# Performance work log

Hardware: AMD Instinct MI355X
Metric: run time of the kernel (lower is better)

## Reference

```python
import jax, jax.numpy as jnp
import numpy as np

MIN_POS = 1e-6
EPS = 1e-20
B, S, F_IN, E, H = 2, 1024, 768, 768, 12
DH = E // H   # nnmf in_features per head (64)
FH = E // H   # nnmf out_features per head (hidden_features=embed_dim default)
N_NNMF_ITERS = 3
N_ALPHA_ITERS = 3


def l1norm(x, axis=-1):
    # F.normalize(x, p=1, dim=axis, eps=1e-20) for non-negative x
    return x / jnp.maximum(jnp.sum(jnp.abs(x), axis=axis, keepdims=True), EPS)


def setup_inputs() -> dict:
    key = jax.random.key(0)
    k = jax.random.split(key, 6)
    return {
        "x": jax.random.normal(k[0], (B, S, F_IN), jnp.float32),
        "embed_w": jax.random.normal(k[1], (E, F_IN), jnp.float32) * 0.02,
        "embed_b": jnp.zeros((E,), jnp.float32),
        "nnmf_w": jax.random.uniform(k[2], (FH, DH), jnp.float32),  # non-negative NMF dictionary
        "out_w": jax.random.normal(k[3], (F_IN, E), jnp.float32) * 0.02,
        "out_b": jnp.zeros((F_IN,), jnp.float32),
    }


def reference(x, embed_w, embed_b, nnmf_w, out_w, out_b):
    # normalize NMF weight rows (p=1 over in_features), as nnmf_layer.normalize_weights
    W = nnmf_w / jnp.maximum(jnp.sum(nnmf_w, axis=1, keepdims=True), EPS)  # [FH, DH]

    # embed + clamp positive, split heads
    xe = jnp.clip(x @ embed_w.T + embed_b, MIN_POS)            # [B,S,E]
    xe = xe.reshape(B, S, H, DH)                                # [B,S,H,DH]

    # NNMFDense: prepared_input = l1-normalized input (normalize_input_dim=-1)
    inp = l1norm(xe)                                            # [B,S,H,DH]
    h = l1norm(jnp.ones((B, S, H, FH), x.dtype))                # init hidden
    rec = inp
    for _ in range(N_NNMF_ITERS):
        rec = l1norm(jnp.clip(h @ W, MIN_POS))                  # reconstruction [B,S,H,DH]
        h = l1norm(jnp.clip(h * ((inp / rec) @ W.T), MIN_POS))  # multiplicative update

    # normalize_h (p=1, dim=-1)
    h = l1norm(h)                                               # [B,S,H,FH] -> 'bohf'

    # alpha dynamics fixed point
    alpha = jnp.ones((B, H, S, S), x.dtype)                     # 'bhoi'
    h_rec_input = rec * inp                                     # [B,S,H,DH]
    for _ in range(N_ALPHA_ITERS):
        h_mixed = jnp.einsum('bohf,bhoi->bihf', h, alpha)       # [B,S,H,FH]
        arec_inv = 1.0 / (h_mixed @ W + EPS)                    # _reconstruct -> [B,S,H,DH]
        alpha = alpha * jnp.einsum('bohf,bihf->bhoi', h_rec_input, arec_inv)

    out = jnp.einsum('bohf,bhoi->bihf', h, alpha)               # [B,S,H,FH]
    out = out.reshape(B, S, E)                                  # flatten heads
    return out @ out_w.T + out_b                                # out_project
```

## Files before the change

### kernel.cpp

```cpp
#include <hip/hip_runtime.h>

#define B_  2
#define S_  1024
#define FIN 768
#define E_  768
#define H_  12
#define DH  64

typedef unsigned int uint;
typedef unsigned short ushort;
typedef __attribute__((ext_vector_type(8))) short short8;
typedef __attribute__((ext_vector_type(4))) float floatx4;

__device__ __forceinline__ ushort f2bf(float f) {
    uint u = __float_as_uint(f);
    return (ushort)((u + 0x7fffu + ((u >> 16) & 1u)) >> 16);
}

__device__ __forceinline__ uint4 pack8(const ushort* p) {
    uint4 r;
    r.x = (uint)p[0] | ((uint)p[1] << 16);
    r.y = (uint)p[2] | ((uint)p[3] << 16);
    r.z = (uint)p[4] | ((uint)p[5] << 16);
    r.w = (uint)p[6] | ((uint)p[7] << 16);
    return r;
}

__device__ __forceinline__ void split8v(float4 a, float4 b, short8& hi, short8& lo) {
    float v[8] = {a.x, a.y, a.z, a.w, b.x, b.y, b.z, b.w};
    ushort h[8], l[8];
#pragma unroll
    for (int j = 0; j < 8; ++j) {
        h[j] = f2bf(v[j]);
        l[j] = f2bf(v[j] - __uint_as_float(((uint)h[j]) << 16));
    }
    uint4 H = pack8(h), L = pack8(l);
    hi = *(short8*)&H;
    lo = *(short8*)&L;
}

__global__ __launch_bounds__(256) void k_embed_prep(const float* __restrict__ xs,
                                                    const float* __restrict__ ew,
                                                    const float* __restrict__ eb,
                                                    const float* __restrict__ nw,
                                                    float* __restrict__ Wn,
                                                    float* __restrict__ WnT,
                                                    float* __restrict__ r1inv,
                                                    float* __restrict__ zbase,
                                                    float* __restrict__ inp) {
    __shared__ __align__(16) unsigned char smem[28160];
    const int tid = threadIdx.x;
    const int bid = blockIdx.x;

    if (bid >= 768) {
        const int pb = bid - 768;
        if (pb == 0) {
            float* Wl = (float*)smem;
            const int f = tid >> 2, q = tid & 3;
            float v[16];
            float s = 0.f;
#pragma unroll
            for (int i = 0; i < 16; ++i) { v[i] = nw[f * 64 + q * 16 + i]; s += v[i]; }
            s += __shfl_xor(s, 1, 64);
            s += __shfl_xor(s, 2, 64);
            const float inv = 1.f / fmaxf(s, 1e-20f);
#pragma unroll
            for (int i = 0; i < 16; ++i) {
                float w = v[i] * inv;
                Wn[f * 64 + q * 16 + i] = w;
                WnT[(q * 16 + i) * 64 + f] = w;
                Wl[f * 65 + q * 16 + i] = w;
            }
            __syncthreads();
            if (tid < 64) {
                float cs = 0.f;
                for (int ff = 0; ff < 64; ++ff) cs += Wl[ff * 65 + tid];
                float t = fmaxf(cs * (1.f / 64.f), 1e-6f);
                float S = t;
#pragma unroll
                for (int m = 1; m < 64; m <<= 1) S += __shfl_xor(S, m, 64);
                S = fmaxf(S, 1e-20f);
                r1inv[tid] = S / t;
            }
        } else {
            const int i = (pb - 1) * 1024 + tid * 4;
            if (i < 26112) {
                float4 z = make_float4(0.f, 0.f, 0.f, 0.f);
                *(float4*)(zbase + i) = z;
            }
        }
        return;
    }

    const int head = bid % 12;
    const int tok0 = (bid / 12) * 32;
    ushort* As_hi = (ushort*)smem;
    ushort* As_lo = As_hi + 32 * 72;
    ushort* Bs_hi = As_lo + 32 * 72;
    ushort* Bs_lo = Bs_hi + 64 * 72;
    float*  RS    = (float*)(Bs_lo + 64 * 72);

    const int wv = tid >> 6, lane = tid & 63;
    const int mbase = (wv >> 1) * 16;
    const int nbase = (wv & 1) * 32;
    const int lm = lane & 15, lq = lane >> 4;

    floatx4 acc[2];
    acc[0] = (floatx4)0.f;
    acc[1] = (floatx4)0.f;

    const int arow = tid >> 3, akc = (tid & 7) * 8;
    const int brow = tid >> 2, bkq = (tid & 3) * 16;
    const float* xrow = xs + (size_t)(tok0 + arow) * FIN + akc;
    const float* wrg  = ew + (size_t)(head * 64 + brow) * FIN + bkq;

    float4 pa[2], pb[4];
#pragma unroll
    for (int c = 0; c < 2; ++c) pa[c] = *(const float4*)(xrow + c * 4);
#pragma unroll
    for (int c = 0; c < 4; ++c) pb[c] = *(const float4*)(wrg + c * 4);

    for (int kb = 0; kb < FIN; kb += 64) {
        __syncthreads();
        {
            ushort ah[8], al[8], bh[16], bl[16];
            float va[8] = {pa[0].x, pa[0].y, pa[0].z, pa[0].w,
                           pa[1].x, pa[1].y, pa[1].z, pa[1].w};
#pragma unroll
            for (int j = 0; j < 8; ++j) {
                ah[j] = f2bf(va[j]);
                al[j] = f2bf(va[j] - __uint_as_float(((uint)ah[j]) << 16));
            }
#pragma unroll
            for (int c4 = 0; c4 < 4; ++c4) {
                float vb[4] = {pb[c4].x, pb[c4].y, pb[c4].z, pb[c4].w};
#pragma unroll
                for (int j = 0; j < 4; ++j) {
                    ushort g = f2bf(vb[j]);
                    bh[c4 * 4 + j] = g;
                    bl[c4 * 4 + j] = f2bf(vb[j] - __uint_as_float(((uint)g) << 16));
                }
            }
            const int aoff = arow * 72 + akc;
            *(uint4*)&As_hi[aoff] = pack8(ah);
            *(uint4*)&As_lo[aoff] = pack8(al);
            const int boff = brow * 72 + bkq;
            *(uint4*)&Bs_hi[boff]     = pack8(bh);
            *(uint4*)&Bs_hi[boff + 8] = pack8(bh + 8);
            *(uint4*)&Bs_lo[boff]     = pack8(bl);
            *(uint4*)&Bs_lo[boff + 8] = pack8(bl + 8);
        }
        __syncthreads();
        if (kb + 64 < FIN) {
#pragma unroll
            for (int c = 0; c < 2; ++c) pa[c] = *(const float4*)(xrow + kb + 64 + c * 4);
#pragma unroll
            for (int c = 0; c < 4; ++c) pb[c] = *(const float4*)(wrg + kb + 64 + c * 4);
        }
#pragma unroll
        for (int ch = 0; ch < 2; ++ch) {
            const int ko = ch * 32 + lq * 8;
            short8 ah = *(const short8*)&As_hi[(mbase + lm) * 72 + ko];
            short8 al = *(const short8*)&As_lo[(mbase + lm) * 72 + ko];
#pragma unroll
            for (int ti = 0; ti < 2; ++ti) {
                short8 bh = *(const short8*)&Bs_hi[(nbase + ti * 16 + lm) * 72 + ko];
                short8 bl = *(const short8*)&Bs_lo[(nbase + ti * 16 + lm) * 72 + ko];
                acc[ti] = __builtin_amdgcn_mfma_f32_16x16x32_bf16(ah, bh, acc[ti], 0, 0, 0);
                acc[ti] = __builtin_amdgcn_mfma_f32_16x16x32_bf16(al, bh, acc[ti], 0, 0, 0);
                acc[ti] = __builtin_amdgcn_mfma_f32_16x16x32_bf16(ah, bl, acc[ti], 0, 0, 0);
            }
        }
    }

    const float b0 = eb[head * 64 + nbase + lm];
    const float b1 = eb[head * 64 + nbase + 16 + lm];
    float xe[2][4];
    float rs[4];
#pragma unroll
    for (int r = 0; r < 4; ++r) {
        float e0 = fmaxf(acc[0][r] + b0, 1e-6f);
        float e1 = fmaxf(acc[1][r] + b1, 1e-6f);
        xe[0][r] = e0; xe[1][r] = e1;
        float p = e0 + e1;
        p += __shfl_xor(p, 1, 64);
        p += __shfl_xor(p, 2, 64);
        p += __shfl_xor(p, 4, 64);
        p += __shfl_xor(p, 8, 64);
        rs[r] = p;
    }
    if (lm == 0) {
#pragma unroll
        for (int r = 0; r < 4; ++r)
            RS[(wv & 1) * 32 + mbase + lq * 4 + r] = rs[r];
    }
    __syncthreads();
    const size_t obase = ((size_t)((tok0 >> 10) * 12 + head) * 1024 + (tok0 & 1023));
#pragma unroll
    for (int r = 0; r < 4; ++r) {
        const int m = mbase + lq * 4 + r;
        const float inv = 1.f / fmaxf(RS[m] + RS[32 + m], 1e-20f);
        float* op = inp + (obase + m) * 64;
        op[nbase + lm]      = xe[0][r] * inv;
        op[nbase + 16 + lm] = xe[1][r] * inv;
    }
}

__device__ __forceinline__ void mfma_matvec(const float srcC[4][4], float* T,
                                            int lm, int lq,
                                            const ushort* WH, const ushort* WL,
                                            floatx4 out[4]) {
    __builtin_amdgcn_wave_barrier();
#pragma unroll
    for (int nt = 0; nt < 4; ++nt)
#pragma unroll
        for (int r = 0; r < 4; ++r)
            T[(lq * 4 + r) * 68 + nt * 16 + lm] = srcC[nt][r];
    __builtin_amdgcn_wave_barrier();
    float4 a00 = *(const float4*)&T[lm * 68 + lq * 8];
    float4 a01 = *(const float4*)&T[lm * 68 + lq * 8 + 4];
    float4 a10 = *(const float4*)&T[lm * 68 + 32 + lq * 8];
    float4 a11 = *(const float4*)&T[lm * 68 + 32 + lq * 8 + 4];
    __builtin_amdgcn_wave_barrier();
    short8 A0h, A0l, A1h, A1l;
    split8v(a00, a01, A0h, A0l);
    split8v(a10, a11, A1h, A1l);
#pragma unroll
    for (int nt = 0; nt < 4; ++nt) {
        const int row = (nt * 16 + lm) * 72;
        short8 b0h = *(const short8*)&WH[row + lq * 8];
        short8 b0l = *(const short8*)&WL[row + lq * 8];
        short8 b1h = *(const short8*)&WH[row + 32 + lq * 8];
        short8 b1l = *(const short8*)&WL[row + 32 + lq * 8];
        floatx4 acc = (floatx4)0.f;
        acc = __builtin_amdgcn_mfma_f32_16x16x32_bf16(A0h, b0h, acc, 0, 0, 0);
        acc = __builtin_amdgcn_mfma_f32_16x16x32_bf16(A0l, b0h, acc, 0, 0, 0);
        acc = __builtin_amdgcn_mfma_f32_16x16x32_bf16(A0h, b0l, acc, 0, 0, 0);
        acc = __builtin_amdgcn_mfma_f32_16x16x32_bf16(A1h, b1h, acc, 0, 0, 0);
        acc = __builtin_amdgcn_mfma_f32_16x16x32_bf16(A1l, b1h, acc, 0, 0, 0);
        acc = __builtin_amdgcn_mfma_f32_16x16x32_bf16(A1h, b1l, acc, 0, 0, 0);
        out[nt] = acc;
    }
}

__global__ __launch_bounds__(256) void k_nnmf(const float* __restrict__ inp,
                                              const float* __restrict__ Wn,
                                              const float* __restrict__ WnT,
                                              const float* __restrict__ r1inv,
                                              float* __restrict__ hout,
                                              float* __restrict__ hriout,
                                              float* __restrict__ mp0) {
    __shared__ ushort WtH[64 * 72], WtL[64 * 72];
    __shared__ ushort WwH[64 * 72], WwL[64 * 72];
    __shared__ float Tb[4][16 * 68];
    const int tid = threadIdx.x, wv = tid >> 6, lane = tid & 63;
    const int lm = lane & 15, lq = lane >> 4;
    float* T = Tb[wv];
    const int rowbase = blockIdx.x * 64 + wv * 16;

    {
        const int row = tid >> 2, kq = (tid & 3) * 16;
        short8 h0, l0, h1, l1;
        split8v(*(const float4*)(WnT + row * 64 + kq), *(const float4*)(WnT + row * 64 + kq + 4), h0, l0);
        split8v(*(const float4*)(WnT + row * 64 + kq + 8), *(const float4*)(WnT + row * 64 + kq + 12), h1, l1);
        *(short8*)&WtH[row * 72 + kq] = h0; *(short8*)&WtH[row * 72 + kq + 8] = h1;
        *(short8*)&WtL[row * 72 + kq] = l0; *(short8*)&WtL[row * 72 + kq + 8] = l1;
        split8v(*(const float4*)(Wn + row * 64 + kq), *(const float4*)(Wn + row * 64 + kq + 4), h0, l0);
        split8v(*(const float4*)(Wn + row * 64 + kq + 8), *(const float4*)(Wn + row * 64 + kq + 12), h1, l1);
        *(short8*)&WwH[row * 72 + kq] = h0; *(short8*)&WwH[row * 72 + kq + 8] = h1;
        *(short8*)&WwL[row * 72 + kq] = l0; *(short8*)&WwL[row * 72 + kq + 8] = l1;
    }

    float inpC[4][4];
#pragma unroll
    for (int nt = 0; nt < 4; ++nt)
#pragma unroll
        for (int r = 0; r < 4; ++r)
            inpC[nt][r] = inp[(size_t)(rowbase + lq * 4 + r) * 64 + nt * 16 + lm];
    float r1c[4];
#pragma unroll
    for (int nt = 0; nt < 4; ++nt) r1c[nt] = r1inv[nt * 16 + lm];
    __syncthreads();

    float hC[4][4], recC[4][4];
    {
        float qC[4][4];
#pragma unroll
        for (int nt = 0; nt < 4; ++nt)
#pragma unroll
            for (int r = 0; r < 4; ++r) qC[nt][r] = inpC[nt][r] * r1c[nt];
        floatx4 u[4];
        mfma_matvec(qC, T, lm, lq, WwH, WwL, u);
#pragma unroll
        for (int nt = 0; nt < 4; ++nt)
#pragma unroll
            for (int r = 0; r < 4; ++r)
                hC[nt][r] = fmaxf(u[nt][r] * (1.f / 64.f), 1e-6f);
#pragma unroll
        for (int r = 0; r < 4; ++r) {
            float s = (hC[0][r] + hC[1][r]) + (hC[2][r] + hC[3][r]);
            s += __shfl_xor(s, 1, 64); s += __shfl_xor(s, 2, 64);
            s += __shfl_xor(s, 4, 64); s += __shfl_xor(s, 8, 64);
            const float inv = __builtin_amdgcn_rcpf(fmaxf(s, 1e-20f));
#pragma unroll
            for (int nt = 0; nt < 4; ++nt) hC[nt][r] *= inv;
        }
    }
#pragma unroll 1
    for (int it = 0; it < 2; ++it) {
        floatx4 t[4];
        mfma_matvec(hC, T, lm, lq, WtH, WtL, t);
        float tC[4][4], qC[4][4];
#pragma unroll
        for (int nt = 0; nt < 4; ++nt)
#pragma unroll
            for (int r = 0; r < 4; ++r) tC[nt][r] = fmaxf(t[nt][r], 1e-6f);
#pragma unroll
        for (int r = 0; r < 4; ++r) {
            float s = (tC[0][r] + tC[1][r]) + (tC[2][r] + tC[3][r]);
            s += __shfl_xor(s, 1, 64); s += __shfl_xor(s, 2, 64);
            s += __shfl_xor(s, 4, 64); s += __shfl_xor(s, 8, 64);
            s = fmaxf(s, 1e-20f);
            const float invS = __builtin_amdgcn_rcpf(s);
#pragma unroll
            for (int nt = 0; nt < 4; ++nt) {
                recC[nt][r] = tC[nt][r] * invS;
                qC[nt][r] = inpC[nt][r] * s * __builtin_amdgcn_rcpf(tC[nt][r]);
            }
        }
        floatx4 u[4];
        mfma_matvec(qC, T, lm, lq, WwH, WwL, u);
#pragma unroll
        for (int nt = 0; nt < 4; ++nt)
#pragma unroll
            for (int r = 0; r < 4; ++r)
                hC[nt][r] = fmaxf(hC[nt][r] * u[nt][r], 1e-6f);
#pragma unroll
        for (int r = 0; r < 4; ++r) {
            float s = (hC[0][r] + hC[1][r]) + (hC[2][r] + hC[3][r]);
            s += __shfl_xor(s, 1, 64); s += __shfl_xor(s, 2, 64);
            s += __shfl_xor(s, 4, 64); s += __shfl_xor(s, 8, 64);
            const float inv = __builtin_amdgcn_rcpf(fmaxf(s, 1e-20f));
#pragma unroll
            for (int nt = 0; nt < 4; ++nt) hC[nt][r] *= inv;
        }
    }
#pragma unroll
    for (int r = 0; r < 4; ++r) {
        float s = (hC[0][r] + hC[1][r]) + (hC[2][r] + hC[3][r]);
        s += __shfl_xor(s, 1, 64); s += __shfl_xor(s, 2, 64);
        s += __shfl_xor(s, 4, 64); s += __shfl_xor(s, 8, 64);
        const float inv = __builtin_amdgcn_rcpf(fmaxf(s, 1e-20f));
#pragma unroll
        for (int nt = 0; nt < 4; ++nt) hC[nt][r] *= inv;
    }
#pragma unroll
    for (int nt = 0; nt < 4; ++nt)
#pragma unroll
        for (int r = 0; r < 4; ++r) {
            const size_t o = (size_t)(rowbase + lq * 4 + r) * 64 + nt * 16 + lm;
            hout[o] = hC[nt][r];
            hriout[o] = recC[nt][r] * inpC[nt][r];
        }
    float hs[4];
#pragma unroll
    for (int nt = 0; nt < 4; ++nt) {
        float s = (hC[nt][0] + hC[nt][1]) + (hC[nt][2] + hC[nt][3]);
        s += __shfl_xor(s, 16, 64);
        s += __shfl_xor(s, 32, 64);
        hs[nt] = s;
    }
    float mvv = lq == 0 ? hs[0] : lq == 1 ? hs[1] : lq == 2 ? hs[2] : hs[3];
    atomicAdd(&mp0[(size_t)blockIdx.x * 64 + lq * 16 + lm], mvv);
}

__global__ __launch_bounds__(256) void k_alpha_step(const float* __restrict__ hin,
                                                    const float* __restrict__ hri,
                                                    const float* __restrict__ Wn,
                                                    const float* __restrict__ mp_in,
                                                    float* __restrict__ mp_out,
                                                    float* __restrict__ c,
                                                    float* __restrict__ M,
                                                    int it) {
    __shared__ float mred[4][64];
    __shared__ float mv[64];
    __shared__ float vv[64];
    __shared__ float cl[64];
    const int tid = threadIdx.x;
    const int bh = blockIdx.x >> 4;
    const int chunk = blockIdx.x & 15;
    const size_t rowbase = (size_t)bh * 1024 + chunk * 64;

    {
        int f = tid & 63, p = tid >> 6;
        float s = 0.f;
#pragma unroll
        for (int pp = 0; pp < 4; ++pp)
            s += mp_in[((size_t)bh * 16 + p * 4 + pp) * 64 + f];
        mred[p][f] = s;
    }
    __syncthreads();
    if (tid < 64)
        mv[tid] = (mred[0][tid] + mred[1][tid]) + (mred[2][tid] + mred[3][tid]);
    __syncthreads();
    {
        int d = tid & 63, qq = tid >> 6;
        float r = 0.f;
#pragma unroll
        for (int ff = 0; ff < 16; ++ff)
            r = fmaf(mv[qq * 16 + ff], Wn[(size_t)(qq * 16 + ff) * 64 + d], r);
        mred[qq][d] = r;
    }
    __syncthreads();
    if (tid < 64)
        vv[tid] = 1.f / (((mred[0][tid] + mred[1][tid]) + (mred[2][tid] + mred[3][tid])) + 1e-20f);
    __syncthreads();
    {
        int o = tid >> 2, dq = tid & 3;
        const float* rp = hri + (rowbase + o) * 64 + dq * 16;
        float dot = 0.f;
#pragma unroll
        for (int t4 = 0; t4 < 16; t4 += 4) {
            float4 r4 = *(const float4*)(rp + t4);
            dot = fmaf(r4.x, vv[dq * 16 + t4 + 0], dot);
            dot = fmaf(r4.y, vv[dq * 16 + t4 + 1], dot);
            dot = fmaf(r4.z, vv[dq * 16 + t4 + 2], dot);
            dot = fmaf(r4.w, vv[dq * 16 + t4 + 3], dot);
        }
        dot += __shfl_xor(dot, 1, 64);
        dot += __shfl_xor(dot, 2, 64);
        float cn = dot;
        if (it >= 2) cn *= c[rowbase + o];
        if (dq == 0) { c[rowbase + o] = cn; cl[o] = cn; }
    }
    __syncthreads();
    {
        const int f4 = (tid & 15) * 4, ogr = tid >> 4;
        float4 a = make_float4(0.f, 0.f, 0.f, 0.f);
#pragma unroll
        for (int oi = 0; oi < 4; ++oi) {
            int o = ogr * 4 + oi;
            float4 h4 = *(const float4*)(hin + (rowbase + o) * 64 + f4);
            float cv = cl[o];
            a.x = fmaf(h4.x, cv, a.x); a.y = fmaf(h4.y, cv, a.y);
            a.z = fmaf(h4.z, cv, a.z); a.w = fmaf(h4.w, cv, a.w);
        }
        a.x += __shfl_xor(a.x, 16, 64); a.y += __shfl_xor(a.y, 16, 64);
        a.z += __shfl_xor(a.z, 16, 64); a.w += __shfl_xor(a.w, 16, 64);
        a.x += __shfl_xor(a.x, 32, 64); a.y += __shfl_xor(a.y, 32, 64);
        a.z += __shfl_xor(a.z, 32, 64); a.w += __shfl_xor(a.w, 32, 64);
        const int w = tid >> 6;
        if ((tid & 63) < 16) *(float4*)&mred[w][(tid & 15) * 4] = a;
    }
    __syncthreads();
    if (tid < 64) {
        float s = (mred[0][tid] + mred[1][tid]) + (mred[2][tid] + mred[3][tid]);
        if (it == 3) atomicAdd(&M[(size_t)bh * 64 + tid], s);
        else mp_out[((size_t)bh * 16 + chunk) * 64 + tid] = s;
    }
}

__global__ __launch_bounds__(256) void k_projbcast(const float* __restrict__ M,
                                                   const float* __restrict__ ow,
                                                   const float* __restrict__ ob,
                                                   float* __restrict__ out) {
    __shared__ float Ml[768];
    __shared__ float ps[4][64];
    __shared__ float yseg[64];
    const int tid = threadIdx.x;
    const int b = blockIdx.x / 192;
    const int rem = blockIdx.x - b * 192;
    const int jt = rem >> 4, rg = rem & 15;
    for (int i = tid; i < 768; i += 256) Ml[i] = M[b * 768 + i];
    __syncthreads();
    const int jj = tid & 63, part = tid >> 6;
    const int j = jt * 64 + jj;
    const float* row = ow + (size_t)j * 768 + part * 192;
    float acc = 0.f;
    for (int t = 0; t < 192; t += 4) {
        float4 w4 = *(const float4*)(row + t);
        acc = fmaf(w4.x, Ml[part * 192 + t + 0], acc);
        acc = fmaf(w4.y, Ml[part * 192 + t + 1], acc);
        acc = fmaf(w4.z, Ml[part * 192 + t + 2], acc);
        acc = fmaf(w4.w, Ml[part * 192 + t + 3], acc);
    }
    ps[part][jj] = acc;
    __syncthreads();
    if (tid < 64)
        yseg[tid] = ps[0][tid] + ps[1][tid] + ps[2][tid] + ps[3][tid] + ob[jt * 64 + tid];
    __syncthreads();
    const int r0 = tid >> 2, c4 = (tid & 3) * 16;
    float4 v4[4];
#pragma unroll
    for (int q = 0; q < 4; ++q) v4[q] = *(const float4*)&yseg[c4 + q * 4];
    float* dst = out + ((size_t)(b * 1024 + rg * 64 + r0)) * 768 + jt * 64 + c4;
#pragma unroll
    for (int q = 0; q < 4; ++q) *(float4*)(dst + q * 4) = v4[q];
}

extern "C" void kernel_launch(void* const* d_in, const int* in_sizes, int n_in,
                              void* d_out, int out_size, void* d_ws, size_t ws_size,
                              hipStream_t stream) {
    const float* xs = (const float*)d_in[0];
    const float* ew = (const float*)d_in[1];
    const float* eb = (const float*)d_in[2];
    const float* nw = (const float*)d_in[3];
    const float* ow = (const float*)d_in[4];
    const float* ob = (const float*)d_in[5];
    float* out = (float*)d_out;

    float* ws    = (float*)d_ws;
    float* inp   = ws;
    float* h     = ws + 1572864;
    float* hri   = ws + 3145728;
    float* Wn    = ws + 4718592;
    float* WnT   = ws + 4722688;
    float* r1inv = ws + 4726784;
    float* mp0   = ws + 4727040;
    float* M     = ws + 4751616;
    float* mp1   = ws + 4753152;
    float* mp2   = ws + 4777728;
    float* c     = ws + 4802304;

    k_embed_prep<<<795, 256, 0, stream>>>(xs, ew, eb, nw, Wn, WnT, r1inv, mp0, inp);
    k_nnmf<<<384, 256, 0, stream>>>(inp, Wn, WnT, r1inv, h, hri, mp0);
    k_alpha_step<<<384, 256, 0, stream>>>(h, hri, Wn, mp0, mp1, c, M, 1);
    k_alpha_step<<<384, 256, 0, stream>>>(h, hri, Wn, mp1, mp2, c, M, 2);
    k_alpha_step<<<384, 256, 0, stream>>>(h, hri, Wn, mp2, mp1, c, M, 3);
    k_projbcast<<<384, 256, 0, stream>>>(M, ow, ob, out);
}
```

Measured before the change: 132.0 us.

## Fuse three alpha-step launches into one per-head kernel with transposed h layout

```diff
diff --git a/kernel.cpp b/kernel.cpp
--- a/kernel.cpp
+++ b/kernel.cpp
@@ -46,48 +46,38 @@
                                                     float* __restrict__ Wn,
                                                     float* __restrict__ WnT,
                                                     float* __restrict__ r1inv,
-                                                    float* __restrict__ zbase,
                                                     float* __restrict__ inp) {
     __shared__ __align__(16) unsigned char smem[28160];
     const int tid = threadIdx.x;
     const int bid = blockIdx.x;
 
     if (bid >= 768) {
-        const int pb = bid - 768;
-        if (pb == 0) {
-            float* Wl = (float*)smem;
-            const int f = tid >> 2, q = tid & 3;
-            float v[16];
-            float s = 0.f;
-#pragma unroll
-            for (int i = 0; i < 16; ++i) { v[i] = nw[f * 64 + q * 16 + i]; s += v[i]; }
-            s += __shfl_xor(s, 1, 64);
-            s += __shfl_xor(s, 2, 64);
-            const float inv = 1.f / fmaxf(s, 1e-20f);
-#pragma unroll
-            for (int i = 0; i < 16; ++i) {
-                float w = v[i] * inv;
-                Wn[f * 64 + q * 16 + i] = w;
-                WnT[(q * 16 + i) * 64 + f] = w;
-                Wl[f * 65 + q * 16 + i] = w;
-            }
-            __syncthreads();
-            if (tid < 64) {
-                float cs = 0.f;
-                for (int ff = 0; ff < 64; ++ff) cs += Wl[ff * 65 + tid];
-                float t = fmaxf(cs * (1.f / 64.f), 1e-6f);
-                float S = t;
-#pragma unroll
-                for (int m = 1; m < 64; m <<= 1) S += __shfl_xor(S, m, 64);
-                S = fmaxf(S, 1e-20f);
-                r1inv[tid] = S / t;
-            }
-        } else {
-            const int i = (pb - 1) * 1024 + tid * 4;
-            if (i < 26112) {
-                float4 z = make_float4(0.f, 0.f, 0.f, 0.f);
-                *(float4*)(zbase + i) = z;
-            }
+        float* Wl = (float*)smem;
+        const int f = tid >> 2, q = tid & 3;
+        float v[16];
+        float s = 0.f;
+#pragma unroll
+        for (int i = 0; i < 16; ++i) { v[i] = nw[f * 64 + q * 16 + i]; s += v[i]; }
+        s += __shfl_xor(s, 1, 64);
+        s += __shfl_xor(s, 2, 64);
+        const float inv = 1.f / fmaxf(s, 1e-20f);
+#pragma unroll
+        for (int i = 0; i < 16; ++i) {
+            float w = v[i] * inv;
+            Wn[f * 64 + q * 16 + i] = w;
+            WnT[(q * 16 + i) * 64 + f] = w;
+            Wl[f * 65 + q * 16 + i] = w;
+        }
+        __syncthreads();
+        if (tid < 64) {
+            float cs = 0.f;
+            for (int ff = 0; ff < 64; ++ff) cs += Wl[ff * 65 + tid];
+            float t = fmaxf(cs * (1.f / 64.f), 1e-6f);
+            float S = t;
+#pragma unroll
+            for (int m = 1; m < 64; m <<= 1) S += __shfl_xor(S, m, 64);
+            S = fmaxf(S, 1e-20f);
+            r1inv[tid] = S / t;
         }
         return;
     }
@@ -247,8 +237,8 @@
                                               const float* __restrict__ Wn,
                                               const float* __restrict__ WnT,
                                               const float* __restrict__ r1inv,
-                                              float* __restrict__ hout,
-                                              float* __restrict__ hriout,
+                                              float* __restrict__ hT,
+                                              float* __restrict__ hriT,
                                               float* __restrict__ mp0) {
     __shared__ ushort WtH[64 * 72], WtL[64 * 72];
     __shared__ ushort WwH[64 * 72], WwL[64 * 72];
@@ -354,14 +344,7 @@
 #pragma unroll
         for (int nt = 0; nt < 4; ++nt) hC[nt][r] *= inv;
     }
-#pragma unroll
-    for (int nt = 0; nt < 4; ++nt)
-#pragma unroll
-        for (int r = 0; r < 4; ++r) {
-            const size_t o = (size_t)(rowbase + lq * 4 + r) * 64 + nt * 16 + lm;
-            hout[o] = hC[nt][r];
-            hriout[o] = recC[nt][r] * inpC[nt][r];
-        }
+
     float hs[4];
 #pragma unroll
     for (int nt = 0; nt < 4; ++nt) {
@@ -370,93 +353,131 @@
         s += __shfl_xor(s, 32, 64);
         hs[nt] = s;
     }
-    float mvv = lq == 0 ? hs[0] : lq == 1 ? hs[1] : lq == 2 ? hs[2] : hs[3];
-    atomicAdd(&mp0[(size_t)blockIdx.x * 64 + lq * 16 + lm], mvv);
-}
-
-__global__ __launch_bounds__(256) void k_alpha_step(const float* __restrict__ hin,
-                                                    const float* __restrict__ hri,
-                                                    const float* __restrict__ Wn,
-                                                    const float* __restrict__ mp_in,
-                                                    float* __restrict__ mp_out,
-                                                    float* __restrict__ c,
-                                                    float* __restrict__ M,
-                                                    int it) {
-    __shared__ float mred[4][64];
-    __shared__ float mv[64];
-    __shared__ float vv[64];
-    __shared__ float cl[64];
-    const int tid = threadIdx.x;
-    const int bh = blockIdx.x >> 4;
-    const int chunk = blockIdx.x & 15;
-    const size_t rowbase = (size_t)bh * 1024 + chunk * 64;
-
-    {
-        int f = tid & 63, p = tid >> 6;
+
+    __syncthreads();
+    float* TBh = (float*)WwH;
+    float* TBr = (float*)WtH;
+    float* pbuf = (float*)Tb;
+#pragma unroll
+    for (int nt = 0; nt < 4; ++nt)
+#pragma unroll
+        for (int r = 0; r < 4; ++r) {
+            const int ol = wv * 16 + lq * 4 + r, f = nt * 16 + lm;
+            TBh[ol * 65 + f] = hC[nt][r];
+            TBr[ol * 65 + f] = recC[nt][r] * inpC[nt][r];
+        }
+    pbuf[wv * 64 + lq * 16 + lm] = hs[lq];
+    __syncthreads();
+    const int bh = blockIdx.x >> 4, obase = (blockIdx.x & 15) * 64;
+    float* hTb  = hT   + (size_t)bh * 64 * 1024 + obase;
+    float* rTb  = hriT + (size_t)bh * 64 * 1024 + obase;
+#pragma unroll
+    for (int p = 0; p < 16; ++p) {
+        const int f = wv * 16 + p;
+        hTb[(size_t)f * 1024 + lane] = TBh[lane * 65 + f];
+        rTb[(size_t)f * 1024 + lane] = TBr[lane * 65 + f];
+    }
+    if (tid < 64) {
+        float tot = (pbuf[tid] + pbuf[64 + tid]) + (pbuf[128 + tid] + pbuf[192 + tid]);
+        mp0[(size_t)blockIdx.x * 64 + tid] = tot;
+    }
+}
+
+__global__ __launch_bounds__(1024) void k_alpha(const float* __restrict__ hT,
+                                                const float* __restrict__ hriT,
+                                                const float* __restrict__ Wn,
+                                                const float* __restrict__ mp0,
+                                                float* __restrict__ M) {
+    __shared__ float red[16 * 64];
+    __shared__ float mvl[64];
+    __shared__ float vvl[64];
+    __shared__ float cl[1024];
+    const int tid = threadIdx.x, bh = blockIdx.x;
+    const int w = tid >> 6, lane = tid & 63;
+    const float* hTb = hT   + (size_t)bh * 64 * 1024;
+    const float* rTb = hriT + (size_t)bh * 64 * 1024;
+
+    float rT[64];
+#pragma unroll
+    for (int f = 0; f < 64; ++f) rT[f] = rTb[(size_t)f * 1024 + tid];
+    float wcol[4];
+#pragma unroll
+    for (int j = 0; j < 4; ++j) wcol[j] = Wn[(size_t)(w * 4 + j) * 64 + lane];
+
+    float c = 1.f;
+#pragma unroll 1
+    for (int it = 1; it <= 3; ++it) {
+        if (it == 1) {
+            red[tid] = mp0[((size_t)bh * 16 + w) * 64 + lane];
+            __syncthreads();
+            if (tid < 64) {
+                float s = 0.f;
+#pragma unroll
+                for (int cc = 0; cc < 16; ++cc) s += red[cc * 64 + tid];
+                mvl[tid] = s;
+            }
+        } else {
+#pragma unroll
+            for (int j = 0; j < 4; ++j) {
+                const int f = w * 4 + j;
+                const float* hrow = hTb + (size_t)f * 1024;
+                float s = 0.f;
+#pragma unroll
+                for (int k = 0; k < 4; ++k) {
+                    const float4 hv = *(const float4*)(hrow + lane * 4 + k * 256);
+                    const float4 cv = *(const float4*)&cl[lane * 4 + k * 256];
+                    s = fmaf(hv.x, cv.x, s); s = fmaf(hv.y, cv.y, s);
+                    s = fmaf(hv.z, cv.z, s); s = fmaf(hv.w, cv.w, s);
+                }
+                s += __shfl_xor(s, 1, 64);  s += __shfl_xor(s, 2, 64);
+                s += __shfl_xor(s, 4, 64);  s += __shfl_xor(s, 8, 64);
+                s += __shfl_xor(s, 16, 64); s += __shfl_xor(s, 32, 64);
+                if (lane == 0) mvl[f] = s;
+            }
+        }
+        __syncthreads();
+        {
+            float r = 0.f;
+#pragma unroll
+            for (int j = 0; j < 4; ++j) r = fmaf(mvl[w * 4 + j], wcol[j], r);
+            red[tid] = r;
+        }
+        __syncthreads();
+        if (tid < 64) {
+            float s = 0.f;
+#pragma unroll
+            for (int cc = 0; cc < 16; ++cc) s += red[cc * 64 + tid];
+            vvl[tid] = 1.f / (s + 1e-20f);
+        }
+        __syncthreads();
+        float d0 = 0.f, d1 = 0.f, d2 = 0.f, d3 = 0.f;
+#pragma unroll
+        for (int f = 0; f < 64; f += 4) {
+            d0 = fmaf(rT[f + 0], vvl[f + 0], d0);
+            d1 = fmaf(rT[f + 1], vvl[f + 1], d1);
+            d2 = fmaf(rT[f + 2], vvl[f + 2], d2);
+            d3 = fmaf(rT[f + 3], vvl[f + 3], d3);
+        }
+        c *= ((d0 + d1) + (d2 + d3));
+        cl[tid] = c;
+        __syncthreads();
+    }
+#pragma unroll
+    for (int j = 0; j < 4; ++j) {
+        const int f = w * 4 + j;
+        const float* hrow = hTb + (size_t)f * 1024;
         float s = 0.f;
 #pragma unroll
-        for (int pp = 0; pp < 4; ++pp)
-            s += mp_in[((size_t)bh * 16 + p * 4 + pp) * 64 + f];
-        mred[p][f] = s;
-    }
-    __syncthreads();
-    if (tid < 64)
-        mv[tid] = (mred[0][tid] + mred[1][tid]) + (mred[2][tid] + mred[3][tid]);
-    __syncthreads();
-    {
-        int d = tid & 63, qq = tid >> 6;
-        float r = 0.f;
-#pragma unroll
-        for (int ff = 0; ff < 16; ++ff)
-            r = fmaf(mv[qq * 16 + ff], Wn[(size_t)(qq * 16 + ff) * 64 + d], r);
-        mred[qq][d] = r;
-    }
-    __syncthreads();
-    if (tid < 64)
-        vv[tid] = 1.f / (((mred[0][tid] + mred[1][tid]) + (mred[2][tid] + mred[3][tid])) + 1e-20f);
-    __syncthreads();
-    {
-        int o = tid >> 2, dq = tid & 3;
-        const float* rp = hri + (rowbase + o) * 64 + dq * 16;
-        float dot = 0.f;
-#pragma unroll
-        for (int t4 = 0; t4 < 16; t4 += 4) {
-            float4 r4 = *(const float4*)(rp + t4);
-            dot = fmaf(r4.x, vv[dq * 16 + t4 + 0], dot);
-            dot = fmaf(r4.y, vv[dq * 16 + t4 + 1], dot);
-            dot = fmaf(r4.z, vv[dq * 16 + t4 + 2], dot);
-            dot = fmaf(r4.w, vv[dq * 16 + t4 + 3], dot);
-        }
-        dot += __shfl_xor(dot, 1, 64);
-        dot += __shfl_xor(dot, 2, 64);
-        float cn = dot;
-        if (it >= 2) cn *= c[rowbase + o];
-        if (dq == 0) { c[rowbase + o] = cn; cl[o] = cn; }
-    }
-    __syncthreads();
-    {
-        const int f4 = (tid & 15) * 4, ogr = tid >> 4;
-        float4 a = make_float4(0.f, 0.f, 0.f, 0.f);
-#pragma unroll
-        for (int oi = 0; oi < 4; ++oi) {
-            int o = ogr * 4 + oi;
-            float4 h4 = *(const float4*)(hin + (rowbase + o) * 64 + f4);
-            float cv = cl[o];
-            a.x = fmaf(h4.x, cv, a.x); a.y = fmaf(h4.y, cv, a.y);
-            a.z = fmaf(h4.z, cv, a.z); a.w = fmaf(h4.w, cv, a.w);
-        }
-        a.x += __shfl_xor(a.x, 16, 64); a.y += __shfl_xor(a.y, 16, 64);
-        a.z += __shfl_xor(a.z, 16, 64); a.w += __shfl_xor(a.w, 16, 64);
-        a.x += __shfl_xor(a.x, 32, 64); a.y += __shfl_xor(a.y, 32, 64);
-        a.z += __shfl_xor(a.z, 32, 64); a.w += __shfl_xor(a.w, 32, 64);
-        const int w = tid >> 6;
-        if ((tid & 63) < 16) *(float4*)&mred[w][(tid & 15) * 4] = a;
-    }
-    __syncthreads();
-    if (tid < 64) {
-        float s = (mred[0][tid] + mred[1][tid]) + (mred[2][tid] + mred[3][tid]);
-        if (it == 3) atomicAdd(&M[(size_t)bh * 64 + tid], s);
-        else mp_out[((size_t)bh * 16 + chunk) * 64 + tid] = s;
+        for (int k = 0; k < 4; ++k) {
+            const float4 hv = *(const float4*)(hrow + lane * 4 + k * 256);
+            const float4 cv = *(const float4*)&cl[lane * 4 + k * 256];
+            s = fmaf(hv.x, cv.x, s); s = fmaf(hv.y, cv.y, s);
+            s = fmaf(hv.z, cv.z, s); s = fmaf(hv.w, cv.w, s);
+        }
+        s += __shfl_xor(s, 1, 64);  s += __shfl_xor(s, 2, 64);
+        s += __shfl_xor(s, 4, 64);  s += __shfl_xor(s, 8, 64);
+        s += __shfl_xor(s, 16, 64); s += __shfl_xor(s, 32, 64);
+        if (lane == 0) M[(size_t)bh * 64 + f] = s;
     }
 }
 
@@ -511,21 +532,16 @@
 
     float* ws    = (float*)d_ws;
     float* inp   = ws;
-    float* h     = ws + 1572864;
-    float* hri   = ws + 3145728;
+    float* hT    = ws + 1572864;
+    float* hriT  = ws + 3145728;
     float* Wn    = ws + 4718592;
     float* WnT   = ws + 4722688;
     float* r1inv = ws + 4726784;
     float* mp0   = ws + 4727040;
     float* M     = ws + 4751616;
-    float* mp1   = ws + 4753152;
-    float* mp2   = ws + 4777728;
-    float* c     = ws + 4802304;
-
-    k_embed_prep<<<795, 256, 0, stream>>>(xs, ew, eb, nw, Wn, WnT, r1inv, mp0, inp);
-    k_nnmf<<<384, 256, 0, stream>>>(inp, Wn, WnT, r1inv, h, hri, mp0);
-    k_alpha_step<<<384, 256, 0, stream>>>(h, hri, Wn, mp0, mp1, c, M, 1);
-    k_alpha_step<<<384, 256, 0, stream>>>(h, hri, Wn, mp1, mp2, c, M, 2);
-    k_alpha_step<<<384, 256, 0, stream>>>(h, hri, Wn, mp2, mp1, c, M, 3);
+
+    k_embed_prep<<<769, 256, 0, stream>>>(xs, ew, eb, nw, Wn, WnT, r1inv, inp);
+    k_nnmf<<<384, 256, 0, stream>>>(inp, Wn, WnT, r1inv, hT, hriT, mp0);
+    k_alpha<<<24, 1024, 0, stream>>>(hT, hriT, Wn, mp0, M);
     k_projbcast<<<384, 256, 0, stream>>>(M, ow, ob, out);
 }
```

Result: slower. 137.5 us (+4.1%).

## Replace atomics and zero-init with deterministic partial sums; split MFMA accumulators

Applied to the files above, without the earlier changes.

```diff
diff --git a/kernel.cpp b/kernel.cpp
--- a/kernel.cpp
+++ b/kernel.cpp
@@ -46,48 +46,38 @@
                                                     float* __restrict__ Wn,
                                                     float* __restrict__ WnT,
                                                     float* __restrict__ r1inv,
-                                                    float* __restrict__ zbase,
                                                     float* __restrict__ inp) {
     __shared__ __align__(16) unsigned char smem[28160];
     const int tid = threadIdx.x;
     const int bid = blockIdx.x;
 
     if (bid >= 768) {
-        const int pb = bid - 768;
-        if (pb == 0) {
-            float* Wl = (float*)smem;
-            const int f = tid >> 2, q = tid & 3;
-            float v[16];
-            float s = 0.f;
-#pragma unroll
-            for (int i = 0; i < 16; ++i) { v[i] = nw[f * 64 + q * 16 + i]; s += v[i]; }
-            s += __shfl_xor(s, 1, 64);
-            s += __shfl_xor(s, 2, 64);
-            const float inv = 1.f / fmaxf(s, 1e-20f);
-#pragma unroll
-            for (int i = 0; i < 16; ++i) {
-                float w = v[i] * inv;
-                Wn[f * 64 + q * 16 + i] = w;
-                WnT[(q * 16 + i) * 64 + f] = w;
-                Wl[f * 65 + q * 16 + i] = w;
-            }
-            __syncthreads();
-            if (tid < 64) {
-                float cs = 0.f;
-                for (int ff = 0; ff < 64; ++ff) cs += Wl[ff * 65 + tid];
-                float t = fmaxf(cs * (1.f / 64.f), 1e-6f);
-                float S = t;
-#pragma unroll
-                for (int m = 1; m < 64; m <<= 1) S += __shfl_xor(S, m, 64);
-                S = fmaxf(S, 1e-20f);
-                r1inv[tid] = S / t;
-            }
-        } else {
-            const int i = (pb - 1) * 1024 + tid * 4;
-            if (i < 26112) {
-                float4 z = make_float4(0.f, 0.f, 0.f, 0.f);
-                *(float4*)(zbase + i) = z;
-            }
+        float* Wl = (float*)smem;
+        const int f = tid >> 2, q = tid & 3;
+        float v[16];
+        float s = 0.f;
+#pragma unroll
+        for (int i = 0; i < 16; ++i) { v[i] = nw[f * 64 + q * 16 + i]; s += v[i]; }
+        s += __shfl_xor(s, 1, 64);
+        s += __shfl_xor(s, 2, 64);
+        const float inv = 1.f / fmaxf(s, 1e-20f);
+#pragma unroll
+        for (int i = 0; i < 16; ++i) {
+            float w = v[i] * inv;
+            Wn[f * 64 + q * 16 + i] = w;
+            WnT[(q * 16 + i) * 64 + f] = w;
+            Wl[f * 65 + q * 16 + i] = w;
+        }
+        __syncthreads();
+        if (tid < 64) {
+            float cs = 0.f;
+            for (int ff = 0; ff < 64; ++ff) cs += Wl[ff * 65 + tid];
+            float t = fmaxf(cs * (1.f / 64.f), 1e-6f);
+            float S = t;
+#pragma unroll
+            for (int m = 1; m < 64; m <<= 1) S += __shfl_xor(S, m, 64);
+            S = fmaxf(S, 1e-20f);
+            r1inv[tid] = S / t;
         }
         return;
     }
@@ -105,9 +95,9 @@
     const int nbase = (wv & 1) * 32;
     const int lm = lane & 15, lq = lane >> 4;
 
-    floatx4 acc[2];
-    acc[0] = (floatx4)0.f;
-    acc[1] = (floatx4)0.f;
+    floatx4 accA[2], accB[2];
+    accA[0] = (floatx4)0.f; accA[1] = (floatx4)0.f;
+    accB[0] = (floatx4)0.f; accB[1] = (floatx4)0.f;
 
     const int arow = tid >> 3, akc = (tid & 7) * 8;
     const int brow = tid >> 2, bkq = (tid & 3) * 16;
@@ -123,32 +113,18 @@
     for (int kb = 0; kb < FIN; kb += 64) {
         __syncthreads();
         {
-            ushort ah[8], al[8], bh[16], bl[16];
-            float va[8] = {pa[0].x, pa[0].y, pa[0].z, pa[0].w,
-                           pa[1].x, pa[1].y, pa[1].z, pa[1].w};
-#pragma unroll
-            for (int j = 0; j < 8; ++j) {
-                ah[j] = f2bf(va[j]);
-                al[j] = f2bf(va[j] - __uint_as_float(((uint)ah[j]) << 16));
-            }
-#pragma unroll
-            for (int c4 = 0; c4 < 4; ++c4) {
-                float vb[4] = {pb[c4].x, pb[c4].y, pb[c4].z, pb[c4].w};
-#pragma unroll
-                for (int j = 0; j < 4; ++j) {
-                    ushort g = f2bf(vb[j]);
-                    bh[c4 * 4 + j] = g;
-                    bl[c4 * 4 + j] = f2bf(vb[j] - __uint_as_float(((uint)g) << 16));
-                }
-            }
+            short8 Ah, Al, B0h, B0l, B1h, B1l;
+            split8v(pa[0], pa[1], Ah, Al);
+            split8v(pb[0], pb[1], B0h, B0l);
+            split8v(pb[2], pb[3], B1h, B1l);
             const int aoff = arow * 72 + akc;
-            *(uint4*)&As_hi[aoff] = pack8(ah);
-            *(uint4*)&As_lo[aoff] = pack8(al);
+            *(short8*)&As_hi[aoff] = Ah;
+            *(short8*)&As_lo[aoff] = Al;
             const int boff = brow * 72 + bkq;
-            *(uint4*)&Bs_hi[boff]     = pack8(bh);
-            *(uint4*)&Bs_hi[boff + 8] = pack8(bh + 8);
-            *(uint4*)&Bs_lo[boff]     = pack8(bl);
-            *(uint4*)&Bs_lo[boff + 8] = pack8(bl + 8);
+            *(short8*)&Bs_hi[boff]     = B0h;
+            *(short8*)&Bs_hi[boff + 8] = B1h;
+            *(short8*)&Bs_lo[boff]     = B0l;
+            *(short8*)&Bs_lo[boff + 8] = B1l;
         }
         __syncthreads();
         if (kb + 64 < FIN) {
@@ -166,9 +142,9 @@
             for (int ti = 0; ti < 2; ++ti) {
                 short8 bh = *(const short8*)&Bs_hi[(nbase + ti * 16 + lm) * 72 + ko];
                 short8 bl = *(const short8*)&Bs_lo[(nbase + ti * 16 + lm) * 72 + ko];
-                acc[ti] = __builtin_amdgcn_mfma_f32_16x16x32_bf16(ah, bh, acc[ti], 0, 0, 0);
-                acc[ti] = __builtin_amdgcn_mfma_f32_16x16x32_bf16(al, bh, acc[ti], 0, 0, 0);
-                acc[ti] = __builtin_amdgcn_mfma_f32_16x16x32_bf16(ah, bl, acc[ti], 0, 0, 0);
+                accA[ti] = __builtin_amdgcn_mfma_f32_16x16x32_bf16(ah, bh, accA[ti], 0, 0, 0);
+                accB[ti] = __builtin_amdgcn_mfma_f32_16x16x32_bf16(al, bh, accB[ti], 0, 0, 0);
+                accB[ti] = __builtin_amdgcn_mfma_f32_16x16x32_bf16(ah, bl, accB[ti], 0, 0, 0);
             }
         }
     }
@@ -179,8 +155,8 @@
     float rs[4];
 #pragma unroll
     for (int r = 0; r < 4; ++r) {
-        float e0 = fmaxf(acc[0][r] + b0, 1e-6f);
-        float e1 = fmaxf(acc[1][r] + b1, 1e-6f);
+        float e0 = fmaxf((accA[0][r] + accB[0][r]) + b0, 1e-6f);
+        float e1 = fmaxf((accA[1][r] + accB[1][r]) + b1, 1e-6f);
         xe[0][r] = e0; xe[1][r] = e1;
         float p = e0 + e1;
         p += __shfl_xor(p, 1, 64);
@@ -232,14 +208,14 @@
         short8 b0l = *(const short8*)&WL[row + lq * 8];
         short8 b1h = *(const short8*)&WH[row + 32 + lq * 8];
         short8 b1l = *(const short8*)&WL[row + 32 + lq * 8];
-        floatx4 acc = (floatx4)0.f;
-        acc = __builtin_amdgcn_mfma_f32_16x16x32_bf16(A0h, b0h, acc, 0, 0, 0);
-        acc = __builtin_amdgcn_mfma_f32_16x16x32_bf16(A0l, b0h, acc, 0, 0, 0);
-        acc = __builtin_amdgcn_mfma_f32_16x16x32_bf16(A0h, b0l, acc, 0, 0, 0);
-        acc = __builtin_amdgcn_mfma_f32_16x16x32_bf16(A1h, b1h, acc, 0, 0, 0);
-        acc = __builtin_amdgcn_mfma_f32_16x16x32_bf16(A1l, b1h, acc, 0, 0, 0);
-        acc = __builtin_amdgcn_mfma_f32_16x16x32_bf16(A1h, b1l, acc, 0, 0, 0);
-        out[nt] = acc;
+        floatx4 acc0 = (floatx4)0.f, acc1 = (floatx4)0.f;
+        acc0 = __builtin_amdgcn_mfma_f32_16x16x32_bf16(A0h, b0h, acc0, 0, 0, 0);
+        acc0 = __builtin_amdgcn_mfma_f32_16x16x32_bf16(A0l, b0h, acc0, 0, 0, 0);
+        acc0 = __builtin_amdgcn_mfma_f32_16x16x32_bf16(A0h, b0l, acc0, 0, 0, 0);
+        acc1 = __builtin_amdgcn_mfma_f32_16x16x32_bf16(A1h, b1h, acc1, 0, 0, 0);
+        acc1 = __builtin_amdgcn_mfma_f32_16x16x32_bf16(A1l, b1h, acc1, 0, 0, 0);
+        acc1 = __builtin_amdgcn_mfma_f32_16x16x32_bf16(A1h, b1l, acc1, 0, 0, 0);
+        out[nt] = acc0 + acc1;
     }
 }
 
@@ -253,6 +229,7 @@
     __shared__ ushort WtH[64 * 72], WtL[64 * 72];
     __shared__ ushort WwH[64 * 72], WwL[64 * 72];
     __shared__ float Tb[4][16 * 68];
+    __shared__ float pbuf[256];
     const int tid = threadIdx.x, wv = tid >> 6, lane = tid & 63;
     const int lm = lane & 15, lq = lane >> 4;
     float* T = Tb[wv];
@@ -354,6 +331,7 @@
 #pragma unroll
         for (int nt = 0; nt < 4; ++nt) hC[nt][r] *= inv;
     }
+
 #pragma unroll
     for (int nt = 0; nt < 4; ++nt)
 #pragma unroll
@@ -362,6 +340,7 @@
             hout[o] = hC[nt][r];
             hriout[o] = recC[nt][r] * inpC[nt][r];
         }
+
     float hs[4];
 #pragma unroll
     for (int nt = 0; nt < 4; ++nt) {
@@ -370,8 +349,12 @@
         s += __shfl_xor(s, 32, 64);
         hs[nt] = s;
     }
-    float mvv = lq == 0 ? hs[0] : lq == 1 ? hs[1] : lq == 2 ? hs[2] : hs[3];
-    atomicAdd(&mp0[(size_t)blockIdx.x * 64 + lq * 16 + lm], mvv);
+    pbuf[wv * 64 + lq * 16 + lm] = hs[lq];
+    __syncthreads();
+    if (tid < 64) {
+        float tot = (pbuf[tid] + pbuf[64 + tid]) + (pbuf[128 + tid] + pbuf[192 + tid]);
+        mp0[(size_t)blockIdx.x * 64 + tid] = tot;
+    }
 }
 
 __global__ __launch_bounds__(256) void k_alpha_step(const float* __restrict__ hin,
@@ -380,7 +363,6 @@
                                                     const float* __restrict__ mp_in,
                                                     float* __restrict__ mp_out,
                                                     float* __restrict__ c,
-                                                    float* __restrict__ M,
                                                     int it) {
     __shared__ float mred[4][64];
     __shared__ float mv[64];
@@ -455,12 +437,11 @@
     __syncthreads();
     if (tid < 64) {
         float s = (mred[0][tid] + mred[1][tid]) + (mred[2][tid] + mred[3][tid]);
-        if (it == 3) atomicAdd(&M[(size_t)bh * 64 + tid], s);
-        else mp_out[((size_t)bh * 16 + chunk) * 64 + tid] = s;
-    }
-}
-
-__global__ __launch_bounds__(256) void k_projbcast(const float* __restrict__ M,
+        mp_out[((size_t)bh * 16 + chunk) * 64 + tid] = s;
+    }
+}
+
+__global__ __launch_bounds__(256) void k_projbcast(const float* __restrict__ mp3,
                                                    const float* __restrict__ ow,
                                                    const float* __restrict__ ob,
                                                    float* __restrict__ out) {
@@ -471,7 +452,14 @@
     const int b = blockIdx.x / 192;
     const int rem = blockIdx.x - b * 192;
     const int jt = rem >> 4, rg = rem & 15;
-    for (int i = tid; i < 768; i += 256) Ml[i] = M[b * 768 + i];
+    for (int i = tid; i < 768; i += 256) {
+        const int hh = i >> 6, f = i & 63;
+        const float* src = mp3 + ((size_t)(b * 12 + hh) * 16) * 64 + f;
+        float s = 0.f;
+#pragma unroll
+        for (int cc = 0; cc < 16; ++cc) s += src[cc * 64];
+        Ml[i] = s;
+    }
     __syncthreads();
     const int jj = tid & 63, part = tid >> 6;
     const int j = jt * 64 + jj;
@@ -517,15 +505,14 @@
     float* WnT   = ws + 4722688;
     float* r1inv = ws + 4726784;
     float* mp0   = ws + 4727040;
-    float* M     = ws + 4751616;
-    float* mp1   = ws + 4753152;
-    float* mp2   = ws + 4777728;
-    float* c     = ws + 4802304;
-
-    k_embed_prep<<<795, 256, 0, stream>>>(xs, ew, eb, nw, Wn, WnT, r1inv, mp0, inp);
+    float* mp1   = ws + 4751616;
+    float* mp2   = ws + 4776192;
+    float* c     = ws + 4800768;
+
+    k_embed_prep<<<769, 256, 0, stream>>>(xs, ew, eb, nw, Wn, WnT, r1inv, inp);
     k_nnmf<<<384, 256, 0, stream>>>(inp, Wn, WnT, r1inv, h, hri, mp0);
-    k_alpha_step<<<384, 256, 0, stream>>>(h, hri, Wn, mp0, mp1, c, M, 1);
-    k_alpha_step<<<384, 256, 0, stream>>>(h, hri, Wn, mp1, mp2, c, M, 2);
-    k_alpha_step<<<384, 256, 0, stream>>>(h, hri, Wn, mp2, mp1, c, M, 3);
-    k_projbcast<<<384, 256, 0, stream>>>(M, ow, ob, out);
-}
+    k_alpha_step<<<384, 256, 0, stream>>>(h, hri, Wn, mp0, mp1, c, 1);
+    k_alpha_step<<<384, 256, 0, stream>>>(h, hri, Wn, mp1, mp2, c, 2);
+    k_alpha_step<<<384, 256, 0, stream>>>(h, hri, Wn, mp2, mp1, c, 3);
+    k_projbcast<<<384, 256, 0, stream>>>(mp1, ow, ob, out);
+}
```

Result: no change. 133.0 us (+0.8%).
